# Performance work log

Hardware: AMD Instinct MI355X
Metric: run time of the kernel (lower is better)

## Reference

```python
import jax, jax.numpy as jnp
import numpy as np
from jax import lax

N_SAMPLES = 2 ** 15   # 32768
N_ATOMS = 2048
ATOM_SIZE = 1024
K_SPARSE = 64
BATCH = 4


def setup_inputs() -> dict:
    key = jax.random.key(0)
    k1, k2 = jax.random.split(key)
    orig = jax.random.normal(k1, (BATCH, 1, N_SAMPLES), dtype=jnp.float32)
    # atoms ~ uniform(-1, 1) as in the torch Parameter init
    atoms = jax.random.uniform(k2, (N_ATOMS, ATOM_SIZE), dtype=jnp.float32,
                               minval=-1.0, maxval=1.0)
    return {"orig": orig, "atoms": atoms}


def reference(orig, atoms):
    B = orig.shape[0]
    # Correlate input with the atom dictionary (F.conv1d, padding=atom_size//2).
    x = lax.conv_general_dilated(
        orig, atoms.reshape(N_ATOMS, 1, ATOM_SIZE),
        window_strides=(1,), padding=[(ATOM_SIZE // 2, ATOM_SIZE // 2)],
        dimension_numbers=("NCH", "OIH", "NCH"))  # [B, n_atoms, N+1]
    x = x[..., :N_SAMPLES]                          # [B, n_atoms, N]
    # dropout(p=0.05) omitted (eval-mode / deterministic reference)

    # sparsify: per-batch top-k over the flattened (atom, time) grid
    flat = x.reshape(B, N_ATOMS * N_SAMPLES)
    values, indices = lax.top_k(flat, K_SPARSE)      # [B, K]
    atom_idx = indices // N_SAMPLES                  # [B, K]
    time_idx = indices % N_SAMPLES                   # [B, K]

    # Overlap-add synthesis: gather atom, scale, scatter-add into 2N buffer.
    contrib = atoms[atom_idx] * values[..., None]    # [B, K, atom_size]
    pos = time_idx[..., None] + jnp.arange(ATOM_SIZE)  # [B, K, atom_size]
    b_idx = jnp.arange(B)[:, None, None]
    out = jnp.zeros((B, 2 * N_SAMPLES), dtype=orig.dtype)
    out = out.at[b_idx, pos].add(contrib)
    return out[:, None, :N_SAMPLES]                  # [B, 1, N]
```

## Files before the change

kernel.cpp:

```cpp
#include <hip/hip_runtime.h>

#define NS     32768
#define NA     2048
#define ASZ    1024
#define NB     4
#define SIGC   34848
#define BM     128
#define BN     128
#define BK     128
#define TILES  4096
#define CAP    8192
#define MINT   5080
#define SSCALE 20.0f

typedef signed char s8;
typedef __attribute__((ext_vector_type(4))) int i32x4;

__device__ __forceinline__ int imax(int a, int b) { return a > b ? a : b; }

__global__ void prep_atoms_k(const float* __restrict__ atoms, s8* __restrict__ abf,
                             int* __restrict__ wlc) {
  if (blockIdx.x == 0 && threadIdx.x == 0) *wlc = 0;
  int a = blockIdx.x;
  const float* srow = atoms + (size_t)a * ASZ;
  s8* drow = abf + (size_t)a * ASZ;
  for (int k = threadIdx.x; k < ASZ; k += 256) {
    float q = fminf(127.f, fmaxf(-127.f, srow[k] * 127.f));
    drow[k] = (s8)__float2int_rn(q);
  }
}

__global__ void prep_sig_k(const float* __restrict__ orig, s8* __restrict__ sigsh,
                           float* __restrict__ sigf) {
  int i = blockIdx.x * 256 + threadIdx.x;
  if (i >= SIGC) return;
  int b = blockIdx.y >> 4, m = blockIdx.y & 15;
  int j = i + m - 512;
  float f = (j >= 0 && j < NS) ? orig[(size_t)b * NS + j] : 0.0f;
  float q = fminf(127.f, fmaxf(-127.f, f * SSCALE));
  sigsh[(size_t)(b * 16 + m) * SIGC + i] = (s8)__float2int_rn(q);
  if (m == 0) sigf[(size_t)b * SIGC + i] = f;
}

__device__ __forceinline__ void tile_core(const s8* __restrict__ Ab, const s8* __restrict__ Sb,
                                          int t0, s8* Al, s8* Bl, int w, int lane,
                                          i32x4 acc[4][4]) {
  int wr = w >> 1, wc = w & 1;
  int lr = lane >> 3, ls = lane & 7, cs = ls ^ lr;
  int arow = wr * 64 + (lane & 15);
  int brow = wc * 64 + (lane & 15);
  int kgrp = lane >> 4;

  #pragma unroll
  for (int i = 0; i < 4; i++)
    #pragma unroll
    for (int j = 0; j < 4; j++)
      acc[i][j] = (i32x4){0, 0, 0, 0};

  for (int k0 = 0; k0 < ASZ; k0 += BK) {
    #pragma unroll
    for (int i = 0; i < 8; i++) {
      int c = w * 8 + i;
      if (c < 16) {
        const s8* src = Ab + (size_t)(c * 8 + lr) * ASZ + k0 + cs * 16;
        __builtin_amdgcn_global_load_lds((const __attribute__((address_space(1))) void*)src,
            (__attribute__((address_space(3))) void*)(&Al[c * 1024]), 16, 0, 0);
      } else {
        int c2 = c - 16;
        int m = 8 * (c2 & 1) + lr;
        const s8* src = Sb + (size_t)m * SIGC + t0 + 16 * (c2 >> 1) + k0 + cs * 16;
        __builtin_amdgcn_global_load_lds((const __attribute__((address_space(1))) void*)src,
            (__attribute__((address_space(3))) void*)(&Bl[c2 * 1024]), 16, 0, 0);
      }
    }
    __syncthreads();
    #pragma unroll
    for (int kk = 0; kk < 2; kk++) {
      int sl = kk * 4 + kgrp;
      i32x4 af[4], bfr[4];
      #pragma unroll
      for (int mf = 0; mf < 4; mf++) {
        int row = arow + mf * 16;
        af[mf] = *(const i32x4*)&Al[row * BK + ((sl ^ (row & 7)) * 16)];
      }
      #pragma unroll
      for (int nf = 0; nf < 4; nf++) {
        int row = brow + nf * 16;
        bfr[nf] = *(const i32x4*)&Bl[row * BK + ((sl ^ (row & 7)) * 16)];
      }
      #pragma unroll
      for (int mf = 0; mf < 4; mf++)
        #pragma unroll
        for (int nf = 0; nf < 4; nf++)
          acc[mf][nf] = __builtin_amdgcn_mfma_i32_16x16x64_i8(af[mf], bfr[nf], acc[mf][nf], 0, 0, 0);
    }
    __syncthreads();
  }
}

__global__ __launch_bounds__(256, 4)
void screen1(const s8* __restrict__ abf, const s8* __restrict__ sigsh,
             int* __restrict__ tmax)
{
  __shared__ __align__(16) s8 Al[BM * BK];
  __shared__ __align__(16) s8 Bl[BN * BK];
  int bid0 = blockIdx.x;
  int bid  = (bid0 & 7) * ((NB * TILES) >> 3) + (bid0 >> 3);
  int b = bid >> 12, tile = bid & 4095;
  int mt = tile >> 8, nt = tile & 255;
  int m0 = mt * BM, t0 = nt * BN;
  int tid = threadIdx.x, w = tid >> 6, lane = tid & 63;

  i32x4 acc[4][4];
  tile_core(abf + (size_t)m0 * ASZ, sigsh + (size_t)b * 16 * SIGC, t0, Al, Bl, w, lane, acc);

  int lmax = -2147483647;
  #pragma unroll
  for (int mf = 0; mf < 4; mf++)
    #pragma unroll
    for (int nf = 0; nf < 4; nf++)
      #pragma unroll
      for (int q = 0; q < 4; q++) lmax = imax(lmax, acc[mf][nf][q]);
  #pragma unroll
  for (int off = 32; off; off >>= 1) lmax = imax(lmax, __shfl_xor(lmax, off, 64));
  int* wredp = (int*)Al;
  if (lane == 0) wredp[w] = lmax;
  __syncthreads();
  if (tid == 0)
    tmax[b * TILES + tile] = imax(imax(wredp[0], wredp[1]), imax(wredp[2], wredp[3]));
}

__global__ void thresh_k(const int* __restrict__ tmax, int* __restrict__ thr,
                         int* __restrict__ ccnt, int* __restrict__ wl, int* __restrict__ wlc) {
  int b = blockIdx.x, tid = threadIdx.x;
  __shared__ int hist[4096];
  __shared__ int tsum[256];
  __shared__ int hist2[256];
  __shared__ int sB1, sAbove, sThr;
  for (int i = tid; i < 4096; i += 256) hist[i] = 0;
  __syncthreads();
  for (int i = tid; i < TILES; i += 256) {
    unsigned u = (unsigned)tmax[b * TILES + i] ^ 0x80000000u;
    atomicAdd(&hist[u >> 20], 1);
  }
  __syncthreads();
  { int s = 0;
    for (int j = 0; j < 16; j++) s += hist[tid * 16 + j];
    tsum[tid] = s; }
  __syncthreads();
  if (tid == 0) {
    int cum = 0, T = 0;
    for (int t2 = 255; t2 >= 0; t2--) {
      if (cum + tsum[t2] >= 64) { T = t2; break; }
      cum += tsum[t2];
    }
    int B1 = T * 16;
    for (int bk = T * 16 + 15; bk >= T * 16; bk--) {
      if (cum + hist[bk] >= 64) { B1 = bk; break; }
      cum += hist[bk];
    }
    sB1 = B1; sAbove = cum;
  }
  __syncthreads();
  if (tid < 256) hist2[tid] = 0;
  __syncthreads();
  int B1 = sB1;
  for (int i = tid; i < TILES; i += 256) {
    unsigned u = (unsigned)tmax[b * TILES + i] ^ 0x80000000u;
    if ((int)(u >> 20) == B1) atomicAdd(&hist2[(u >> 12) & 255], 1);
  }
  __syncthreads();
  if (tid == 0) {
    int cum = sAbove, B2 = 0;
    for (int z = 255; z >= 0; z--) { cum += hist2[z]; if (cum >= 64) { B2 = z; break; } }
    unsigned ulow = ((unsigned)B1 << 20) | ((unsigned)B2 << 12);
    int t = (int)(ulow ^ 0x80000000u);
    sThr = t; thr[b] = t; ccnt[b] = 0;
  }
  __syncthreads();
  int cut = sThr - MINT;
  for (int i = tid; i < TILES; i += 256)
    if (tmax[b * TILES + i] >= cut) { int p = atomicAdd(wlc, 1); wl[p] = (b << 12) | i; }
}

__global__ __launch_bounds__(256, 4)
void screen2(const s8* __restrict__ abf, const s8* __restrict__ sigsh,
             const int* __restrict__ thr, const int* __restrict__ wl,
             const int* __restrict__ wlc, int* __restrict__ ccnt, int* __restrict__ cidx)
{
  __shared__ __align__(16) s8 Al[BM * BK];
  __shared__ __align__(16) s8 Bl[BN * BK];
  int n = *wlc; if (n > NB * TILES) n = NB * TILES;
  int tid = threadIdx.x, w = tid >> 6, lane = tid & 63;
  int wr = w >> 1, wc = w & 1;
  int kgrp = lane >> 4;

  for (int wi = blockIdx.x; wi < n; wi += gridDim.x) {
    int e = wl[wi];
    int b = e >> 12, tile = e & 4095;
    int cut = thr[b] - MINT;
    int mt = tile >> 8, nt = tile & 255;
    int m0 = mt * BM, t0 = nt * BN;

    i32x4 acc[4][4];
    tile_core(abf + (size_t)m0 * ASZ, sigsh + (size_t)b * 16 * SIGC, t0, Al, Bl, w, lane, acc);

    int rb = m0 + wr * 64 + 4 * kgrp;
    int cb = t0 + wc * 64 + (lane & 15);
    #pragma unroll
    for (int mf = 0; mf < 4; mf++)
      #pragma unroll
      for (int nf = 0; nf < 4; nf++)
        #pragma unroll
        for (int q = 0; q < 4; q++) {
          if (acc[mf][nf][q] >= cut) {
            int a = rb + mf * 16 + q;
            int t = cb + nf * 16;
            int p = atomicAdd(&ccnt[b], 1);
            if (p < CAP) cidx[b * CAP + p] = (a << 15) | t;
          }
        }
  }
}

__global__ void rescore_k(const float* __restrict__ atoms, const float* __restrict__ sigf,
                          const int* __restrict__ ccnt, const int* __restrict__ cidx,
                          float* __restrict__ cval) {
  int nwv = gridDim.x * 4;
  int gw = blockIdx.x * 4 + (threadIdx.x >> 6);
  int lane = threadIdx.x & 63;
  for (int b = 0; b < NB; b++) {
    int cnt = ccnt[b]; if (cnt > CAP) cnt = CAP;
    for (int ci = gw; ci < cnt; ci += nwv) {
      int idx = cidx[b * CAP + ci];
      int a = idx >> 15, t = idx & (NS - 1);
      const float* ap = atoms + (size_t)a * ASZ;
      const float* sp = sigf + (size_t)b * SIGC + t;
      float sum = 0.f;
      #pragma unroll
      for (int j = 0; j < 16; j++) { int k = lane + 64 * j; sum += ap[k] * sp[k]; }
      #pragma unroll
      for (int off = 32; off; off >>= 1) sum += __shfl_xor(sum, off, 64);
      if (lane == 0) cval[b * CAP + ci] = sum;
    }
  }
}

__global__ void select_k(const int* __restrict__ ccnt, const float* __restrict__ cval,
                         const int* __restrict__ cidx, float* __restrict__ sval,
                         int* __restrict__ sidx) {
  int b = blockIdx.x, tid = threadIdx.x;
  int cnt = ccnt[b]; if (cnt > CAP) cnt = CAP;
  __shared__ float lv[2048];
  __shared__ int li[2048];
  for (int ii = 0; ii * 256 < cnt; ii++) {
    int i = ii * 256 + tid;
    float vi = 0.f; int idi = 0; bool act = i < cnt;
    if (act) { vi = cval[b * CAP + i]; idi = cidx[b * CAP + i]; }
    int rank = 0;
    for (int c0 = 0; c0 < cnt; c0 += 2048) {
      int mchunk = cnt - c0; if (mchunk > 2048) mchunk = 2048;
      __syncthreads();
      for (int j = tid; j < mchunk; j += 256) {
        lv[j] = cval[b * CAP + c0 + j];
        li[j] = cidx[b * CAP + c0 + j];
      }
      __syncthreads();
      if (act)
        for (int j = 0; j < mchunk; j++)
          rank += (lv[j] > vi) || (lv[j] == vi && li[j] < idi);
    }
    if (act && rank < 64) { sval[b * 64 + rank] = vi; sidx[b * 64 + rank] = idi; }
  }
}

__global__ void recon_k(const float* __restrict__ atoms, const float* __restrict__ sval,
                        const int* __restrict__ sidx, float* __restrict__ out) {
  int gp = blockIdx.x * 256 + threadIdx.x;
  int b = gp >> 15, p = gp & (NS - 1);
  __shared__ float vv[64];
  __shared__ int ii[64];
  if (threadIdx.x < 64) {
    vv[threadIdx.x] = sval[b * 64 + threadIdx.x];
    ii[threadIdx.x] = sidx[b * 64 + threadIdx.x];
  }
  __syncthreads();
  float acc = 0.f;
  for (int s = 0; s < 64; s++) {
    int idx = ii[s];
    int a = idx >> 15, t = idx & (NS - 1);
    int off = p - t;
    if (off >= 0 && off < ASZ) acc += vv[s] * atoms[(size_t)a * ASZ + off];
  }
  out[gp] = acc;
}

extern "C" void kernel_launch(void* const* d_in, const int* in_sizes, int n_in,
                              void* d_out, int out_size, void* d_ws, size_t ws_size,
                              hipStream_t stream) {
  const float* orig  = (const float*)d_in[0];
  const float* atoms = (const float*)d_in[1];
  float* out = (float*)d_out;
  char* ws = (char*)d_ws;

  s8*    abf   = (s8*)   (ws + 0);
  s8*    sigsh = (s8*)   (ws + 2097152);
  float* sigf  = (float*)(ws + 4327424);
  int*   tmax  = (int*)  (ws + 4884992);
  int*   thr   = (int*)  (ws + 4950528);
  int*   ccnt  = (int*)  (ws + 4950784);
  float* cval  = (float*)(ws + 4951040);
  int*   cidx  = (int*)  (ws + 5082112);
  float* sval  = (float*)(ws + 5213184);
  int*   sidx  = (int*)  (ws + 5214208);
  int*   wl    = (int*)  (ws + 5215232);
  int*   wlc   = (int*)  (ws + 5280768);

  prep_atoms_k<<<NA, 256, 0, stream>>>(atoms, abf, wlc);
  prep_sig_k<<<dim3((SIGC + 255) / 256, NB * 16), 256, 0, stream>>>(orig, sigsh, sigf);
  screen1<<<NB * TILES, 256, 0, stream>>>(abf, sigsh, tmax);
  thresh_k<<<NB, 256, 0, stream>>>(tmax, thr, ccnt, wl, wlc);
  screen2<<<1024, 256, 0, stream>>>(abf, sigsh, thr, wl, wlc, ccnt, cidx);
  rescore_k<<<128, 256, 0, stream>>>(atoms, sigf, ccnt, cidx, cval);
  select_k<<<NB, 256, 0, stream>>>(ccnt, cval, cidx, sval, sidx);
  recon_k<<<out_size / 256, 256, 0, stream>>>(atoms, sval, sidx, out);
}
```

Measured before the change: 316.4 us.

## Enlarge screening GEMM tiles to 256x256 with double-buffered LDS pipeline

```diff
diff --git a/kernel.cpp b/kernel.cpp
--- a/kernel.cpp
+++ b/kernel.cpp
@@ -5,10 +5,12 @@
 #define ASZ    1024
 #define NB     4
 #define SIGC   34848
-#define BM     128
-#define BN     128
+#define BM     256
+#define BN     256
 #define BK     128
-#define TILES  4096
+#define MT     8
+#define NT     128
+#define TILES  1024
 #define CAP    8192
 #define MINT   5080
 #define SSCALE 20.0f
@@ -42,92 +44,112 @@
   if (m == 0) sigf[(size_t)b * SIGC + i] = f;
 }
 
-__device__ __forceinline__ void tile_core(const s8* __restrict__ Ab, const s8* __restrict__ Sb,
-                                          int t0, s8* Al, s8* Bl, int w, int lane,
-                                          i32x4 acc[4][4]) {
-  int wr = w >> 1, wc = w & 1;
+__device__ __forceinline__ void stage_tile(const s8* __restrict__ Ab, const s8* __restrict__ Sb,
+                                           int t0, int k0, s8* Al, s8* Bl, int w, int lane) {
   int lr = lane >> 3, ls = lane & 7, cs = ls ^ lr;
-  int arow = wr * 64 + (lane & 15);
-  int brow = wc * 64 + (lane & 15);
-  int kgrp = lane >> 4;
-
-  #pragma unroll
-  for (int i = 0; i < 4; i++)
-    #pragma unroll
-    for (int j = 0; j < 4; j++)
-      acc[i][j] = (i32x4){0, 0, 0, 0};
-
-  for (int k0 = 0; k0 < ASZ; k0 += BK) {
+  if (w < 4) {
     #pragma unroll
     for (int i = 0; i < 8; i++) {
       int c = w * 8 + i;
-      if (c < 16) {
-        const s8* src = Ab + (size_t)(c * 8 + lr) * ASZ + k0 + cs * 16;
-        __builtin_amdgcn_global_load_lds((const __attribute__((address_space(1))) void*)src,
-            (__attribute__((address_space(3))) void*)(&Al[c * 1024]), 16, 0, 0);
-      } else {
-        int c2 = c - 16;
-        int m = 8 * (c2 & 1) + lr;
-        const s8* src = Sb + (size_t)m * SIGC + t0 + 16 * (c2 >> 1) + k0 + cs * 16;
-        __builtin_amdgcn_global_load_lds((const __attribute__((address_space(1))) void*)src,
-            (__attribute__((address_space(3))) void*)(&Bl[c2 * 1024]), 16, 0, 0);
-      }
-    }
-    __syncthreads();
-    #pragma unroll
-    for (int kk = 0; kk < 2; kk++) {
-      int sl = kk * 4 + kgrp;
-      i32x4 af[4], bfr[4];
-      #pragma unroll
-      for (int mf = 0; mf < 4; mf++) {
-        int row = arow + mf * 16;
-        af[mf] = *(const i32x4*)&Al[row * BK + ((sl ^ (row & 7)) * 16)];
-      }
-      #pragma unroll
-      for (int nf = 0; nf < 4; nf++) {
-        int row = brow + nf * 16;
-        bfr[nf] = *(const i32x4*)&Bl[row * BK + ((sl ^ (row & 7)) * 16)];
-      }
-      #pragma unroll
-      for (int mf = 0; mf < 4; mf++)
-        #pragma unroll
-        for (int nf = 0; nf < 4; nf++)
-          acc[mf][nf] = __builtin_amdgcn_mfma_i32_16x16x64_i8(af[mf], bfr[nf], acc[mf][nf], 0, 0, 0);
-    }
-    __syncthreads();
-  }
-}
-
-__global__ __launch_bounds__(256, 4)
+      const s8* src = Ab + (size_t)(c * 8 + lr) * ASZ + k0 + cs * 16;
+      __builtin_amdgcn_global_load_lds((const __attribute__((address_space(1))) void*)src,
+          (__attribute__((address_space(3))) void*)(&Al[c * 1024]), 16, 0, 0);
+    }
+  } else {
+    #pragma unroll
+    for (int i = 0; i < 8; i++) {
+      int c2 = (w - 4) * 8 + i;
+      int m = 8 * (c2 & 1) + lr;
+      const s8* src = Sb + (size_t)m * SIGC + t0 + 16 * (c2 >> 1) + k0 + cs * 16;
+      __builtin_amdgcn_global_load_lds((const __attribute__((address_space(1))) void*)src,
+          (__attribute__((address_space(3))) void*)(&Bl[c2 * 1024]), 16, 0, 0);
+    }
+  }
+}
+
+__device__ __forceinline__ void compute_tile(const s8* Al, const s8* Bl, int w, int lane,
+                                             i32x4 acc[8][4]) {
+  int wr = w >> 2, wc = w & 3;
+  int arow0 = wr * 128 + (lane & 15);
+  int brow0 = wc * 64 + (lane & 15);
+  int kgrp = lane >> 4;
+  #pragma unroll
+  for (int kk = 0; kk < 2; kk++) {
+    int sl = kk * 4 + kgrp;
+    i32x4 af[8], bfr[4];
+    #pragma unroll
+    for (int nf = 0; nf < 4; nf++) {
+      int row = brow0 + nf * 16;
+      bfr[nf] = *(const i32x4*)&Bl[row * BK + ((sl ^ (row & 7)) * 16)];
+    }
+    #pragma unroll
+    for (int mf = 0; mf < 8; mf++) {
+      int row = arow0 + mf * 16;
+      af[mf] = *(const i32x4*)&Al[row * BK + ((sl ^ (row & 7)) * 16)];
+    }
+    __builtin_amdgcn_s_setprio(1);
+    #pragma unroll
+    for (int mf = 0; mf < 8; mf++)
+      #pragma unroll
+      for (int nf = 0; nf < 4; nf++)
+        acc[mf][nf] = __builtin_amdgcn_mfma_i32_16x16x64_i8(af[mf], bfr[nf], acc[mf][nf], 0, 0, 0);
+    __builtin_amdgcn_s_setprio(0);
+  }
+}
+
+#define K_PIPELINE(Ab, Sb, t0)                                            \
+  stage_tile(Ab, Sb, t0, 0, Al[0], Bl[0], w, lane);                       \
+  __syncthreads();                                                        \
+  for (int kt = 0; kt < 8; kt += 2) {                                     \
+    stage_tile(Ab, Sb, t0, (kt + 1) * BK, Al[1], Bl[1], w, lane);         \
+    compute_tile(Al[0], Bl[0], w, lane, acc);                             \
+    __syncthreads();                                                      \
+    if (kt + 2 < 8) stage_tile(Ab, Sb, t0, (kt + 2) * BK, Al[0], Bl[0], w, lane); \
+    compute_tile(Al[1], Bl[1], w, lane, acc);                             \
+    __syncthreads();                                                      \
+  }
+
+__global__ __launch_bounds__(512, 2)
 void screen1(const s8* __restrict__ abf, const s8* __restrict__ sigsh,
              int* __restrict__ tmax)
 {
-  __shared__ __align__(16) s8 Al[BM * BK];
-  __shared__ __align__(16) s8 Bl[BN * BK];
+  __shared__ __align__(16) s8 Al[2][BM * BK];
+  __shared__ __align__(16) s8 Bl[2][BN * BK];
+  __shared__ int wred[8];
   int bid0 = blockIdx.x;
   int bid  = (bid0 & 7) * ((NB * TILES) >> 3) + (bid0 >> 3);
-  int b = bid >> 12, tile = bid & 4095;
-  int mt = tile >> 8, nt = tile & 255;
+  int b = bid >> 10, tile = bid & (TILES - 1);
+  int mt = tile >> 7, nt = tile & (NT - 1);
   int m0 = mt * BM, t0 = nt * BN;
   int tid = threadIdx.x, w = tid >> 6, lane = tid & 63;
-
-  i32x4 acc[4][4];
-  tile_core(abf + (size_t)m0 * ASZ, sigsh + (size_t)b * 16 * SIGC, t0, Al, Bl, w, lane, acc);
+  const s8* Ab = abf + (size_t)m0 * ASZ;
+  const s8* Sb = sigsh + (size_t)b * 16 * SIGC;
+
+  i32x4 acc[8][4];
+  #pragma unroll
+  for (int i = 0; i < 8; i++)
+    #pragma unroll
+    for (int j = 0; j < 4; j++) acc[i][j] = (i32x4){0, 0, 0, 0};
+
+  K_PIPELINE(Ab, Sb, t0)
 
   int lmax = -2147483647;
   #pragma unroll
-  for (int mf = 0; mf < 4; mf++)
+  for (int mf = 0; mf < 8; mf++)
     #pragma unroll
     for (int nf = 0; nf < 4; nf++)
       #pragma unroll
       for (int q = 0; q < 4; q++) lmax = imax(lmax, acc[mf][nf][q]);
   #pragma unroll
   for (int off = 32; off; off >>= 1) lmax = imax(lmax, __shfl_xor(lmax, off, 64));
-  int* wredp = (int*)Al;
-  if (lane == 0) wredp[w] = lmax;
-  __syncthreads();
-  if (tid == 0)
-    tmax[b * TILES + tile] = imax(imax(wredp[0], wredp[1]), imax(wredp[2], wredp[3]));
+  if (lane == 0) wred[w] = lmax;
+  __syncthreads();
+  if (tid == 0) {
+    int m = wred[0];
+    #pragma unroll
+    for (int i = 1; i < 8; i++) m = imax(m, wred[i]);
+    tmax[b * TILES + tile] = m;
+  }
 }
 
 __global__ void thresh_k(const int* __restrict__ tmax, int* __restrict__ thr,
@@ -180,35 +202,42 @@
   __syncthreads();
   int cut = sThr - MINT;
   for (int i = tid; i < TILES; i += 256)
-    if (tmax[b * TILES + i] >= cut) { int p = atomicAdd(wlc, 1); wl[p] = (b << 12) | i; }
-}
-
-__global__ __launch_bounds__(256, 4)
+    if (tmax[b * TILES + i] >= cut) { int p = atomicAdd(wlc, 1); wl[p] = (b << 10) | i; }
+}
+
+__global__ __launch_bounds__(512, 2)
 void screen2(const s8* __restrict__ abf, const s8* __restrict__ sigsh,
              const int* __restrict__ thr, const int* __restrict__ wl,
              const int* __restrict__ wlc, int* __restrict__ ccnt, int* __restrict__ cidx)
 {
-  __shared__ __align__(16) s8 Al[BM * BK];
-  __shared__ __align__(16) s8 Bl[BN * BK];
+  __shared__ __align__(16) s8 Al[2][BM * BK];
+  __shared__ __align__(16) s8 Bl[2][BN * BK];
   int n = *wlc; if (n > NB * TILES) n = NB * TILES;
   int tid = threadIdx.x, w = tid >> 6, lane = tid & 63;
-  int wr = w >> 1, wc = w & 1;
+  int wr = w >> 2, wc = w & 3;
   int kgrp = lane >> 4;
 
   for (int wi = blockIdx.x; wi < n; wi += gridDim.x) {
     int e = wl[wi];
-    int b = e >> 12, tile = e & 4095;
+    int b = e >> 10, tile = e & (TILES - 1);
     int cut = thr[b] - MINT;
-    int mt = tile >> 8, nt = tile & 255;
+    int mt = tile >> 7, nt = tile & (NT - 1);
     int m0 = mt * BM, t0 = nt * BN;
-
-    i32x4 acc[4][4];
-    tile_core(abf + (size_t)m0 * ASZ, sigsh + (size_t)b * 16 * SIGC, t0, Al, Bl, w, lane, acc);
-
-    int rb = m0 + wr * 64 + 4 * kgrp;
+    const s8* Ab = abf + (size_t)m0 * ASZ;
+    const s8* Sb = sigsh + (size_t)b * 16 * SIGC;
+
+    i32x4 acc[8][4];
+    #pragma unroll
+    for (int i = 0; i < 8; i++)
+      #pragma unroll
+      for (int j = 0; j < 4; j++) acc[i][j] = (i32x4){0, 0, 0, 0};
+
+    K_PIPELINE(Ab, Sb, t0)
+
+    int rb = m0 + wr * 128 + 4 * kgrp;
     int cb = t0 + wc * 64 + (lane & 15);
     #pragma unroll
-    for (int mf = 0; mf < 4; mf++)
+    for (int mf = 0; mf < 8; mf++)
       #pragma unroll
       for (int nf = 0; nf < 4; nf++)
         #pragma unroll
@@ -220,6 +249,7 @@
             if (p < CAP) cidx[b * CAP + p] = (a << 15) | t;
           }
         }
+    __syncthreads();
   }
 }
 
@@ -307,20 +337,20 @@
   s8*    sigsh = (s8*)   (ws + 2097152);
   float* sigf  = (float*)(ws + 4327424);
   int*   tmax  = (int*)  (ws + 4884992);
-  int*   thr   = (int*)  (ws + 4950528);
-  int*   ccnt  = (int*)  (ws + 4950784);
-  float* cval  = (float*)(ws + 4951040);
-  int*   cidx  = (int*)  (ws + 5082112);
-  float* sval  = (float*)(ws + 5213184);
-  int*   sidx  = (int*)  (ws + 5214208);
-  int*   wl    = (int*)  (ws + 5215232);
-  int*   wlc   = (int*)  (ws + 5280768);
+  int*   thr   = (int*)  (ws + 4901376);
+  int*   ccnt  = (int*)  (ws + 4901632);
+  float* cval  = (float*)(ws + 4901888);
+  int*   cidx  = (int*)  (ws + 5032960);
+  float* sval  = (float*)(ws + 5164032);
+  int*   sidx  = (int*)  (ws + 5165056);
+  int*   wl    = (int*)  (ws + 5166080);
+  int*   wlc   = (int*)  (ws + 5182464);
 
   prep_atoms_k<<<NA, 256, 0, stream>>>(atoms, abf, wlc);
   prep_sig_k<<<dim3((SIGC + 255) / 256, NB * 16), 256, 0, stream>>>(orig, sigsh, sigf);
-  screen1<<<NB * TILES, 256, 0, stream>>>(abf, sigsh, tmax);
+  screen1<<<NB * TILES, 512, 0, stream>>>(abf, sigsh, tmax);
   thresh_k<<<NB, 256, 0, stream>>>(tmax, thr, ccnt, wl, wlc);
-  screen2<<<1024, 256, 0, stream>>>(abf, sigsh, thr, wl, wlc, ccnt, cidx);
+  screen2<<<256, 512, 0, stream>>>(abf, sigsh, thr, wl, wlc, ccnt, cidx);
   rescore_k<<<128, 256, 0, stream>>>(atoms, sigf, ccnt, cidx, cval);
   select_k<<<NB, 256, 0, stream>>>(ccnt, cval, cidx, sval, sidx);
   recon_k<<<out_size / 256, 256, 0, stream>>>(atoms, sval, sidx, out);
```

New measurement: 513.3 us. +62.2%, slower.

## Double-buffer LDS tiles in int8 screening GEMMs and fuse prep kernels

Applied to the files above, without the earlier changes.

```diff
diff --git a/kernel.cpp b/kernel.cpp
--- a/kernel.cpp
+++ b/kernel.cpp
@@ -18,101 +18,118 @@
 
 __device__ __forceinline__ int imax(int a, int b) { return a > b ? a : b; }
 
-__global__ void prep_atoms_k(const float* __restrict__ atoms, s8* __restrict__ abf,
-                             int* __restrict__ wlc) {
+__global__ void prep_k(const float* __restrict__ atoms, const float* __restrict__ orig,
+                       s8* __restrict__ abf, s8* __restrict__ sigsh,
+                       float* __restrict__ sigf, int* __restrict__ wlc) {
   if (blockIdx.x == 0 && threadIdx.x == 0) *wlc = 0;
-  int a = blockIdx.x;
-  const float* srow = atoms + (size_t)a * ASZ;
-  s8* drow = abf + (size_t)a * ASZ;
-  for (int k = threadIdx.x; k < ASZ; k += 256) {
-    float q = fminf(127.f, fmaxf(-127.f, srow[k] * 127.f));
-    drow[k] = (s8)__float2int_rn(q);
-  }
-}
-
-__global__ void prep_sig_k(const float* __restrict__ orig, s8* __restrict__ sigsh,
-                           float* __restrict__ sigf) {
-  int i = blockIdx.x * 256 + threadIdx.x;
-  if (i >= SIGC) return;
-  int b = blockIdx.y >> 4, m = blockIdx.y & 15;
-  int j = i + m - 512;
-  float f = (j >= 0 && j < NS) ? orig[(size_t)b * NS + j] : 0.0f;
-  float q = fminf(127.f, fmaxf(-127.f, f * SSCALE));
-  sigsh[(size_t)(b * 16 + m) * SIGC + i] = (s8)__float2int_rn(q);
-  if (m == 0) sigf[(size_t)b * SIGC + i] = f;
-}
-
-__device__ __forceinline__ void tile_core(const s8* __restrict__ Ab, const s8* __restrict__ Sb,
-                                          int t0, s8* Al, s8* Bl, int w, int lane,
-                                          i32x4 acc[4][4]) {
+  if (blockIdx.x < NA) {
+    int a = blockIdx.x;
+    const float* srow = atoms + (size_t)a * ASZ;
+    s8* drow = abf + (size_t)a * ASZ;
+    for (int k = threadIdx.x; k < ASZ; k += 256) {
+      float q = fminf(127.f, fmaxf(-127.f, srow[k] * 127.f));
+      drow[k] = (s8)__float2int_rn(q);
+    }
+  } else {
+    int r = blockIdx.x - NA;
+    int nch = (SIGC + 255) / 256;
+    int bm = r / nch, chunk = r % nch;
+    int i = chunk * 256 + threadIdx.x;
+    if (i >= SIGC) return;
+    int b = bm >> 4, m = bm & 15;
+    int j = i + m - 512;
+    float f = (j >= 0 && j < NS) ? orig[(size_t)b * NS + j] : 0.0f;
+    float q = fminf(127.f, fmaxf(-127.f, f * SSCALE));
+    sigsh[(size_t)bm * SIGC + i] = (s8)__float2int_rn(q);
+    if (m == 0) sigf[(size_t)b * SIGC + i] = f;
+  }
+}
+
+__device__ __forceinline__ void stage_tile(const s8* __restrict__ Ab, const s8* __restrict__ Sb,
+                                           int t0, int k0, s8* Al, s8* Bl, int w, int lane) {
+  int lr = lane >> 3, ls = lane & 7, cs = ls ^ lr;
+  #pragma unroll
+  for (int i = 0; i < 8; i++) {
+    int c = w * 8 + i;
+    if (c < 16) {
+      const s8* src = Ab + (size_t)(c * 8 + lr) * ASZ + k0 + cs * 16;
+      __builtin_amdgcn_global_load_lds((const __attribute__((address_space(1))) void*)src,
+          (__attribute__((address_space(3))) void*)(&Al[c * 1024]), 16, 0, 0);
+    } else {
+      int c2 = c - 16;
+      int m = 8 * (c2 & 1) + lr;
+      const s8* src = Sb + (size_t)m * SIGC + t0 + 16 * (c2 >> 1) + k0 + cs * 16;
+      __builtin_amdgcn_global_load_lds((const __attribute__((address_space(1))) void*)src,
+          (__attribute__((address_space(3))) void*)(&Bl[c2 * 1024]), 16, 0, 0);
+    }
+  }
+}
+
+__device__ __forceinline__ void compute_tile(const s8* Al, const s8* Bl, int w, int lane,
+                                             i32x4 acc[4][4]) {
   int wr = w >> 1, wc = w & 1;
-  int lr = lane >> 3, ls = lane & 7, cs = ls ^ lr;
-  int arow = wr * 64 + (lane & 15);
-  int brow = wc * 64 + (lane & 15);
+  int arow0 = wr * 64 + (lane & 15);
+  int brow0 = wc * 64 + (lane & 15);
   int kgrp = lane >> 4;
-
-  #pragma unroll
-  for (int i = 0; i < 4; i++)
-    #pragma unroll
-    for (int j = 0; j < 4; j++)
-      acc[i][j] = (i32x4){0, 0, 0, 0};
-
-  for (int k0 = 0; k0 < ASZ; k0 += BK) {
-    #pragma unroll
-    for (int i = 0; i < 8; i++) {
-      int c = w * 8 + i;
-      if (c < 16) {
-        const s8* src = Ab + (size_t)(c * 8 + lr) * ASZ + k0 + cs * 16;
-        __builtin_amdgcn_global_load_lds((const __attribute__((address_space(1))) void*)src,
-            (__attribute__((address_space(3))) void*)(&Al[c * 1024]), 16, 0, 0);
-      } else {
-        int c2 = c - 16;
-        int m = 8 * (c2 & 1) + lr;
-        const s8* src = Sb + (size_t)m * SIGC + t0 + 16 * (c2 >> 1) + k0 + cs * 16;
-        __builtin_amdgcn_global_load_lds((const __attribute__((address_space(1))) void*)src,
-            (__attribute__((address_space(3))) void*)(&Bl[c2 * 1024]), 16, 0, 0);
-      }
-    }
-    __syncthreads();
-    #pragma unroll
-    for (int kk = 0; kk < 2; kk++) {
-      int sl = kk * 4 + kgrp;
-      i32x4 af[4], bfr[4];
-      #pragma unroll
-      for (int mf = 0; mf < 4; mf++) {
-        int row = arow + mf * 16;
-        af[mf] = *(const i32x4*)&Al[row * BK + ((sl ^ (row & 7)) * 16)];
-      }
-      #pragma unroll
-      for (int nf = 0; nf < 4; nf++) {
-        int row = brow + nf * 16;
-        bfr[nf] = *(const i32x4*)&Bl[row * BK + ((sl ^ (row & 7)) * 16)];
-      }
-      #pragma unroll
-      for (int mf = 0; mf < 4; mf++)
-        #pragma unroll
-        for (int nf = 0; nf < 4; nf++)
-          acc[mf][nf] = __builtin_amdgcn_mfma_i32_16x16x64_i8(af[mf], bfr[nf], acc[mf][nf], 0, 0, 0);
-    }
-    __syncthreads();
-  }
-}
-
-__global__ __launch_bounds__(256, 4)
+  #pragma unroll
+  for (int kk = 0; kk < 2; kk++) {
+    int sl = kk * 4 + kgrp;
+    i32x4 af[4], bfr[4];
+    #pragma unroll
+    for (int mf = 0; mf < 4; mf++) {
+      int row = arow0 + mf * 16;
+      af[mf] = *(const i32x4*)&Al[row * BK + ((sl ^ (row & 7)) * 16)];
+    }
+    #pragma unroll
+    for (int nf = 0; nf < 4; nf++) {
+      int row = brow0 + nf * 16;
+      bfr[nf] = *(const i32x4*)&Bl[row * BK + ((sl ^ (row & 7)) * 16)];
+    }
+    __builtin_amdgcn_s_setprio(1);
+    #pragma unroll
+    for (int mf = 0; mf < 4; mf++)
+      #pragma unroll
+      for (int nf = 0; nf < 4; nf++)
+        acc[mf][nf] = __builtin_amdgcn_mfma_i32_16x16x64_i8(af[mf], bfr[nf], acc[mf][nf], 0, 0, 0);
+    __builtin_amdgcn_s_setprio(0);
+  }
+}
+
+#define K_PIPELINE(Ab, Sb, t0)                                                     \
+  stage_tile(Ab, Sb, t0, 0, Al[0], Bl[0], w, lane);                                \
+  __syncthreads();                                                                 \
+  for (int kt = 0; kt < 8; kt += 2) {                                              \
+    stage_tile(Ab, Sb, t0, (kt + 1) * BK, Al[1], Bl[1], w, lane);                  \
+    compute_tile(Al[0], Bl[0], w, lane, acc);                                      \
+    __syncthreads();                                                               \
+    if (kt + 2 < 8) stage_tile(Ab, Sb, t0, (kt + 2) * BK, Al[0], Bl[0], w, lane);  \
+    compute_tile(Al[1], Bl[1], w, lane, acc);                                      \
+    __syncthreads();                                                               \
+  }
+
+__global__ __launch_bounds__(256, 2)
 void screen1(const s8* __restrict__ abf, const s8* __restrict__ sigsh,
              int* __restrict__ tmax)
 {
-  __shared__ __align__(16) s8 Al[BM * BK];
-  __shared__ __align__(16) s8 Bl[BN * BK];
+  __shared__ __align__(16) s8 Al[2][BM * BK];
+  __shared__ __align__(16) s8 Bl[2][BN * BK];
+  __shared__ int wred[4];
   int bid0 = blockIdx.x;
   int bid  = (bid0 & 7) * ((NB * TILES) >> 3) + (bid0 >> 3);
   int b = bid >> 12, tile = bid & 4095;
   int mt = tile >> 8, nt = tile & 255;
   int m0 = mt * BM, t0 = nt * BN;
   int tid = threadIdx.x, w = tid >> 6, lane = tid & 63;
+  const s8* Ab = abf + (size_t)m0 * ASZ;
+  const s8* Sb = sigsh + (size_t)b * 16 * SIGC;
 
   i32x4 acc[4][4];
-  tile_core(abf + (size_t)m0 * ASZ, sigsh + (size_t)b * 16 * SIGC, t0, Al, Bl, w, lane, acc);
+  #pragma unroll
+  for (int i = 0; i < 4; i++)
+    #pragma unroll
+    for (int j = 0; j < 4; j++) acc[i][j] = (i32x4){0, 0, 0, 0};
+
+  K_PIPELINE(Ab, Sb, t0)
 
   int lmax = -2147483647;
   #pragma unroll
@@ -123,11 +140,10 @@
       for (int q = 0; q < 4; q++) lmax = imax(lmax, acc[mf][nf][q]);
   #pragma unroll
   for (int off = 32; off; off >>= 1) lmax = imax(lmax, __shfl_xor(lmax, off, 64));
-  int* wredp = (int*)Al;
-  if (lane == 0) wredp[w] = lmax;
+  if (lane == 0) wred[w] = lmax;
   __syncthreads();
   if (tid == 0)
-    tmax[b * TILES + tile] = imax(imax(wredp[0], wredp[1]), imax(wredp[2], wredp[3]));
+    tmax[b * TILES + tile] = imax(imax(wred[0], wred[1]), imax(wred[2], wred[3]));
 }
 
 __global__ void thresh_k(const int* __restrict__ tmax, int* __restrict__ thr,
@@ -183,13 +199,13 @@
     if (tmax[b * TILES + i] >= cut) { int p = atomicAdd(wlc, 1); wl[p] = (b << 12) | i; }
 }
 
-__global__ __launch_bounds__(256, 4)
+__global__ __launch_bounds__(256, 2)
 void screen2(const s8* __restrict__ abf, const s8* __restrict__ sigsh,
              const int* __restrict__ thr, const int* __restrict__ wl,
              const int* __restrict__ wlc, int* __restrict__ ccnt, int* __restrict__ cidx)
 {
-  __shared__ __align__(16) s8 Al[BM * BK];
-  __shared__ __align__(16) s8 Bl[BN * BK];
+  __shared__ __align__(16) s8 Al[2][BM * BK];
+  __shared__ __align__(16) s8 Bl[2][BN * BK];
   int n = *wlc; if (n > NB * TILES) n = NB * TILES;
   int tid = threadIdx.x, w = tid >> 6, lane = tid & 63;
   int wr = w >> 1, wc = w & 1;
@@ -201,9 +217,16 @@
     int cut = thr[b] - MINT;
     int mt = tile >> 8, nt = tile & 255;
     int m0 = mt * BM, t0 = nt * BN;
+    const s8* Ab = abf + (size_t)m0 * ASZ;
+    const s8* Sb = sigsh + (size_t)b * 16 * SIGC;
 
     i32x4 acc[4][4];
-    tile_core(abf + (size_t)m0 * ASZ, sigsh + (size_t)b * 16 * SIGC, t0, Al, Bl, w, lane, acc);
+    #pragma unroll
+    for (int i = 0; i < 4; i++)
+      #pragma unroll
+      for (int j = 0; j < 4; j++) acc[i][j] = (i32x4){0, 0, 0, 0};
+
+    K_PIPELINE(Ab, Sb, t0)
 
     int rb = m0 + wr * 64 + 4 * kgrp;
     int cb = t0 + wc * 64 + (lane & 15);
@@ -220,6 +243,7 @@
             if (p < CAP) cidx[b * CAP + p] = (a << 15) | t;
           }
         }
+    __syncthreads();
   }
 }
 
@@ -316,11 +340,11 @@
   int*   wl    = (int*)  (ws + 5215232);
   int*   wlc   = (int*)  (ws + 5280768);
 
-  prep_atoms_k<<<NA, 256, 0, stream>>>(atoms, abf, wlc);
-  prep_sig_k<<<dim3((SIGC + 255) / 256, NB * 16), 256, 0, stream>>>(orig, sigsh, sigf);
+  int nch = (SIGC + 255) / 256;
+  prep_k<<<NA + NB * 16 * nch, 256, 0, stream>>>(atoms, orig, abf, sigsh, sigf, wlc);
   screen1<<<NB * TILES, 256, 0, stream>>>(abf, sigsh, tmax);
   thresh_k<<<NB, 256, 0, stream>>>(tmax, thr, ccnt, wl, wlc);
-  screen2<<<1024, 256, 0, stream>>>(abf, sigsh, thr, wl, wlc, ccnt, cidx);
+  screen2<<<512, 256, 0, stream>>>(abf, sigsh, thr, wl, wlc, ccnt, cidx);
   rescore_k<<<128, 256, 0, stream>>>(atoms, sigf, ccnt, cidx, cval);
   select_k<<<NB, 256, 0, stream>>>(ccnt, cval, cidx, sval, sidx);
   recon_k<<<out_size / 256, 256, 0, stream>>>(atoms, sval, sidx, out);
```

Result: slower. 363.3 us (+14.8%).
